# Optimization experiments

Measured on AMD Instinct MI355X. Metric: run time of the kernel, lower is better.

The kernel has to match this reference:

```python
import jax, jax.numpy as jnp
import numpy as np

N = 8192  # nv + nh, bias=False


def setup_inputs() -> dict:
    key = jax.random.key(0)
    k1, k2, k3, k4 = jax.random.split(key, 4)
    w = jax.random.normal(k1, (N, N), dtype=jnp.float32) * 0.01  # learned [n,n] coupling matrix
    initial_state = jax.random.randint(k2, (N,), 0, 2).astype(jnp.float32)  # binary unit states
    clamping_degree = jnp.zeros((N,), dtype=jnp.float32)  # 0 => unit is free to update
    T = jnp.float32(1.0)  # temperature
    perm = jax.random.permutation(k3, N).astype(jnp.int32)  # torch.randperm(self.n)
    rand_u = jax.random.uniform(k4, (N,), dtype=jnp.float32)  # torch.rand(1) per unit
    return {"w": w, "initial_state": initial_state, "clamping_degree": clamping_degree,
            "T": T, "perm": perm, "rand_u": rand_u}


def reference(w, initial_state, clamping_degree, T, perm, rand_u):
    # Sequential Gibbs sweep: for each j in perm, if unclamped,
    # p = sigmoid(w[j]@state / T); state[j] = 1 if u <= p else 0.
    inactive = jnp.float32(0.0)

    def step(state, ju):
        j, u = ju
        sum_input = jnp.dot(w[j], state)          # per-unit dot product against current state
        p = jax.nn.sigmoid(sum_input / T)          # 1/(1+exp(-x/T))
        new_val = jnp.where(u <= p, jnp.float32(1.0), inactive)
        upd = jnp.where(clamping_degree[j] == 0, new_val, state[j])
        return state.at[j].set(upd), None

    final_state, _ = jax.lax.scan(step, initial_state, (perm, rand_u))
    return final_state
```

## Files before the change

### kernel.cpp

```cpp
#include <hip/hip_runtime.h>
#include <math.h>


#define NN 8192
#define BB 512
#define NBLK 16
#define SUB 64
#define NSUB 8
#define NWG 256
#define NWORK 255
#define TPB 512
#define MAXR 3
#define MSTR 68
#define MBUFW (SUB * MSTR)

typedef unsigned int u32;
typedef unsigned long long u64;

__global__ void k_init(u32* flags, int n) {
  int i = blockIdx.x * blockDim.x + threadIdx.x;
  for (; i < n; i += gridDim.x * blockDim.x) flags[i] = 0;
}

__device__ __forceinline__ u32 ld_rlx(const u32* p) {
  return __hip_atomic_load(p, __ATOMIC_RELAXED, __HIP_MEMORY_SCOPE_AGENT);
}
__device__ __forceinline__ void st_rlx(u32* p, u32 v) {
  __hip_atomic_store(p, v, __ATOMIC_RELAXED, __HIP_MEMORY_SCOPE_AGENT);
}
__device__ __forceinline__ float ldf_rlx(const float* p) {
  return __hip_atomic_load(p, __ATOMIC_RELAXED, __HIP_MEMORY_SCOPE_AGENT);
}
__device__ __forceinline__ void stf_rlx(float* p, float v) {
  __hip_atomic_store(p, v, __ATOMIC_RELAXED, __HIP_MEMORY_SCOPE_AGENT);
}
__device__ __forceinline__ double ldd_rlx(const double* p) {
  return __hip_atomic_load(p, __ATOMIC_RELAXED, __HIP_MEMORY_SCOPE_AGENT);
}
__device__ __forceinline__ void std_rlx(double* p, double v) {
  __hip_atomic_store(p, v, __ATOMIC_RELAXED, __HIP_MEMORY_SCOPE_AGENT);
}

__global__ __launch_bounds__(TPB) void k_gibbs(
    const float* __restrict__ w, const float* __restrict__ init,
    const float* __restrict__ clampv, const float* __restrict__ Tp,
    const int* __restrict__ perm, const float* __restrict__ urand,
    float* __restrict__ dout, double* __restrict__ S,
    float* __restrict__ delG, float* __restrict__ tileD,
    u32* delReady, u32* ack) {
  __shared__ double poolD[55296 / 8];
  const int wg = blockIdx.x, tid = threadIdx.x;
  const int wv = tid >> 6, lane = tid & 63;

  if (wg == 0) {
    double* sumsL = poolD;
    double* thrL  = poolD + BB;
    float*  d1L   = (float*)(poolD + 2 * BB);
    float*  d0L   = d1L + BB;
    float*  delL  = d0L + BB;
    float*  oldL  = delL + BB;
    int*    uL    = (int*)(oldL + BB);
    float*  mbuf  = (float*)(uL + BB);

    double T = (double)Tp[0];
    for (int b = 0; b < NBLK; ++b) {
      const bool pub = (b + 1 < NBLK);
      int pos = b * BB + tid;
      int unit = perm[pos];
      double uu = (double)urand[pos];
      thrL[tid] = T * log(uu / (1.0 - uu));
      float old = init[unit];
      bool cl = (clampv[unit] != 0.0f);
      d1L[tid] = cl ? 0.0f : (1.0f - old);
      d0L[tid] = cl ? 0.0f : (0.0f - old);
      oldL[tid] = old;
      uL[tid] = unit;
      {
        const u32* slots = ack + (size_t)b * NWORK;
        for (;;) {
          int ok = 1;
          if (tid < NWORK) ok = (ld_rlx(&slots[tid]) != 0u);
          if (__syncthreads_and(ok)) break;
          __builtin_amdgcn_s_sleep(1);
        }
      }
      sumsL[tid] = ldd_rlx(&S[(size_t)b * BB + tid]);
      if (tid >= 448) {
        int l = tid - 448;
        const float4* src = (const float4*)(tileD + (size_t)b * BB * BB + (size_t)l * BB);
        float4* dst = (float4*)(mbuf + l * MSTR);
#pragma unroll
        for (int j = 0; j < 16; ++j) dst[j] = src[j];
      }
      __syncthreads();
      const float* tb = tileD + (size_t)b * BB * BB;
      float4 nv0, nv1, nv2, nv3;

      for (int t8 = 0; t8 < NSUB; ++t8) {
        int o = t8 * SUB;
        float m[SUB];
        if (tid < SUB) {
          const float4* mr = (const float4*)(mbuf + (t8 & 1) * MBUFW + tid * MSTR);
#pragma unroll
          for (int j = 0; j < 16; ++j) {
            float4 v = mr[j];
            m[4*j] = v.x; m[4*j+1] = v.y; m[4*j+2] = v.z; m[4*j+3] = v.w;
          }
        } else if (t8 > 0 && tid >= 256) {
          int t = tid - 256, g_ = t >> 2, q = t & 3;
          int rrow = o + g_;
          int c0 = (t8 - 1) * SUB + q * 16;
          double p_ =
              (double)(nv0.x * delL[c0])    + (double)(nv0.y * delL[c0+1]) +
              (double)(nv0.z * delL[c0+2])  + (double)(nv0.w * delL[c0+3]) +
              (double)(nv1.x * delL[c0+4])  + (double)(nv1.y * delL[c0+5]) +
              (double)(nv1.z * delL[c0+6])  + (double)(nv1.w * delL[c0+7]);
          p_ +=
              (double)(nv2.x * delL[c0+8])  + (double)(nv2.y * delL[c0+9]) +
              (double)(nv2.z * delL[c0+10]) + (double)(nv2.w * delL[c0+11]) +
              (double)(nv3.x * delL[c0+12]) + (double)(nv3.y * delL[c0+13]) +
              (double)(nv3.z * delL[c0+14]) + (double)(nv3.w * delL[c0+15]);
          p_ += __shfl_down(p_, 2, 4);
          p_ += __shfl_down(p_, 1, 4);
          if (q == 0) sumsL[rrow] += p_;
        }
        __syncthreads();
        if (tid < SUB) {
          float d1v = d1L[o + tid], d0v = d0L[o + tid];
          u64 P1 = __ballot(d1v != 0.0f);
          u64 M0 = __ballot(d0v != 0.0f);
          double g = sumsL[o + tid] - thrL[o + tid];
          u64 xb = 0ull;
          __builtin_amdgcn_s_setprio(3);
#pragma unroll
          for (int s = 0; s < SUB; ++s) {
            u32 t1 = ((P1 >> s) & 1ull) ? 0x3f800000u : 0u;
            u32 t0 = ((M0 >> s) & 1ull) ? 0xbf800000u : 0u;
            int hi = __builtin_amdgcn_readlane(
                (int)(__double_as_longlong(g) >> 32), s);
            float sdf = __uint_as_float((hi >= 0) ? t1 : t0);
            g += (double)(m[s] * sdf);
            xb |= ((u64)(hi >= 0 ? 1 : 0)) << s;
          }
          __builtin_amdgcn_s_setprio(0);
          delL[o + tid] = ((xb >> tid) & 1ull) ? d1v : d0v;
        } else if (tid < 128) {
          if (t8 < NSUB - 1) {
            int l = tid - 64, o2 = (t8 + 1) * SUB;
            const float4* src = (const float4*)(tb + (size_t)(o2 + l) * BB + o2);
            float4* dst = (float4*)(mbuf + ((t8 + 1) & 1) * MBUFW + l * MSTR);
#pragma unroll
            for (int j = 0; j < 16; ++j) dst[j] = src[j];
          }
        } else {
          if (t8 < NSUB - 1 && tid >= 256) {
            int t = tid - 256;
            const float4* pr = (const float4*)(
                tb + (size_t)((t8 + 1) * SUB + (t >> 2)) * BB + o + (t & 3) * 16);
            nv0 = pr[0]; nv1 = pr[1]; nv2 = pr[2]; nv3 = pr[3];
          }
          if (t8 > 0) {
            for (int r = (t8 + 1) * SUB + (tid - 128); r < BB; r += 384) {
              int c0 = (t8 - 1) * SUB;
              const float4* mr3 = (const float4*)(tb + (size_t)r * BB + c0);
              double acc = sumsL[r];
#pragma unroll
              for (int j = 0; j < SUB / 4; ++j) {
                float4 v = mr3[j];
                acc += (double)(v.x * delL[c0+4*j])   + (double)(v.y * delL[c0+4*j+1]) +
                       (double)(v.z * delL[c0+4*j+2]) + (double)(v.w * delL[c0+4*j+3]);
              }
              sumsL[r] = acc;
            }
          }
        }
        __syncthreads();
      }
      if (pub) {
        stf_rlx(&delG[b * BB + tid], delL[tid]);
        __syncthreads();
        if (tid == 0) st_rlx(&delReady[b], 1u);
      }
      dout[uL[tid]] = oldL[tid] + delL[tid];
    }
  } else {
    float* stateL = (float*)poolD;
    double* redW = (double*)((char*)poolD + 32768);
    const int iw = wg - 1;
    const int r0 = (iw * BB) / NWORK, r1 = ((iw + 1) * BB) / NWORK;
    const int cnt = r1 - r0;
    for (int i = tid; i < NN; i += TPB) stateL[i] = init[i];
    __syncthreads();

    for (int p = 0; p < NBLK; ++p) {
      int pc = perm[p * BB + tid];
      float g[NSUB];
      float* tbp = tileD + (size_t)p * BB * BB;

      for (int ri = 0; ri < cnt; ++ri) {
        int unit = perm[p * BB + r0 + ri];
        const float* wrow = w + (size_t)unit * NN;
        const float4* wr4 = (const float4*)wrow;
        const float4* st4 = (const float4*)stateL;
        double acc = 0.0;
#pragma unroll
        for (int k = 0; k < NN / (4 * TPB); ++k) {
          float4 a = wr4[tid + k * TPB];
          float4 s = st4[tid + k * TPB];
          acc += (double)(a.x * s.x) + (double)(a.y * s.y) +
                 (double)(a.z * s.z) + (double)(a.w * s.w);
        }
        for (int o = 32; o > 0; o >>= 1) acc += __shfl_down(acc, o, 64);
        if (lane == 0) redW[wv * MAXR + ri] = acc;
        stf_rlx(&tbp[(size_t)(r0 + ri) * BB + tid], wrow[pc]);
        if (p > 0 && wv == ri) {
#pragma unroll
          for (int t8 = 0; t8 < NSUB; ++t8)
            g[t8] = wrow[perm[(p - 1) * BB + t8 * SUB + lane]];
        }
      }
      __syncthreads();
      double Sr = 0.0;
      if (wv < cnt) {
#pragma unroll
        for (int k = 0; k < TPB / 64; ++k) Sr += redW[k * MAXR + wv];
      }
      if (p > 0) {
        if (tid == 0) {
          while (ld_rlx(&delReady[p - 1]) == 0u) __builtin_amdgcn_s_sleep(1);
        }
        __syncthreads();
        double crr = 0.0;
        if (wv < cnt) {
#pragma unroll
          for (int t8 = 0; t8 < NSUB; ++t8)
            crr += (double)(g[t8] * ldf_rlx(&delG[(p - 1) * BB + t8 * SUB + lane]));
          for (int o = 32; o > 0; o >>= 1) crr += __shfl_down(crr, o, 64);
          Sr += crr;
        }
      }
      if (wv < cnt && lane == 0) std_rlx(&S[(size_t)p * BB + r0 + wv], Sr);
      __syncthreads();
      if (tid == 0) st_rlx(&ack[(size_t)p * NWORK + iw], 1u);
      if (p > 0) {
        float dl = ldf_rlx(&delG[(p - 1) * BB + tid]);
        stateL[perm[(p - 1) * BB + tid]] += dl;
      }
      __syncthreads();
    }
  }
}

extern "C" void kernel_launch(void* const* d_in, const int* in_sizes, int n_in,
                              void* d_out, int out_size, void* d_ws, size_t ws_size,
                              hipStream_t stream) {
  const float* w      = (const float*)d_in[0];
  const float* init   = (const float*)d_in[1];
  const float* clampv = (const float*)d_in[2];
  const float* Tp     = (const float*)d_in[3];
  const int*   perm   = (const int*)d_in[4];
  const float* urand  = (const float*)d_in[5];
  float* dout = (float*)d_out;

  double* S    = (double*)d_ws;
  float* delG  = (float*)(S + (size_t)NBLK * BB);
  float* tileD = delG + NN;
  u32* delReady = (u32*)(tileD + (size_t)NBLK * BB * BB);
  u32* ack      = delReady + NBLK;

  int nflags = NBLK + NBLK * NWORK;
  k_init<<<8, 256, 0, stream>>>(delReady, nflags);

  void* args[] = {(void*)&w, (void*)&init, (void*)&clampv, (void*)&Tp,
                  (void*)&perm, (void*)&urand, (void*)&dout,
                  (void*)&S, (void*)&delG, (void*)&tileD,
                  (void*)&delReady, (void*)&ack};
  hipLaunchCooperativeKernel((const void*)k_gibbs, dim3(NWG), dim3(TPB),
                             args, 0, stream);
}
```

Measured before the change: 589.4 us.

## Publish Gibbs deltas per sub-block and defer last sub-block correction to master

The master workgroup now publishes each 64-unit sub-block of state deltas with its own flag as soon as it is sampled, instead of one flag per 512-unit block. Worker workgroups consume the first seven sub-blocks progressively while computing their corrections. The last sub-block's contribution is handled by the master itself, using a new strip of weights (stripG) that workers write, so workers need not wait for the whole block to finish. This aims to shorten the critical serial dependency between master and workers. The cost is more flag polling and barriers, extra global traffic for the strip, and more complex synchronization.

```diff
diff --git a/kernel.cpp b/kernel.cpp
--- a/kernel.cpp
+++ b/kernel.cpp
@@ -46,8 +46,8 @@
     const float* __restrict__ clampv, const float* __restrict__ Tp,
     const int* __restrict__ perm, const float* __restrict__ urand,
     float* __restrict__ dout, double* __restrict__ S,
-    float* __restrict__ delG, float* __restrict__ tileD,
-    u32* delReady, u32* ack) {
+    float* __restrict__ delG, float* __restrict__ stripG,
+    float* __restrict__ tileD, u32* subFlag, u32* ack) {
   __shared__ double poolD[55296 / 8];
   const int wg = blockIdx.x, tid = threadIdx.x;
   const int wv = tid >> 6, lane = tid & 63;
@@ -55,16 +55,22 @@
   if (wg == 0) {
     double* sumsL = poolD;
     double* thrL  = poolD + BB;
-    float*  d1L   = (float*)(poolD + 2 * BB);
-    float*  d0L   = d1L + BB;
-    float*  delL  = d0L + BB;
-    float*  oldL  = delL + BB;
-    int*    uL    = (int*)(oldL + BB);
-    float*  mbuf  = (float*)(uL + BB);
+    float*  fbase = (float*)(poolD + 2 * BB);
+    float*  d1L   = fbase;
+    float*  d0L   = fbase + BB;
+    float*  delL  = fbase + 2 * BB;
+    float*  oldL  = fbase + 3 * BB;
+    float*  del7L = fbase + 4 * BB;
+    int*    uL    = (int*)(fbase + 4 * BB + SUB);
+    float*  mbuf  = fbase + 4 * BB + SUB + BB;
 
     double T = (double)Tp[0];
+    float4 nv0, nv1, nv2, nv3;
+    float4 sv0, sv1, sv2, sv3;
+
     for (int b = 0; b < NBLK; ++b) {
       const bool pub = (b + 1 < NBLK);
+      if (b > 0 && tid < SUB) del7L[tid] = delL[(NSUB - 1) * SUB + tid];
       int pos = b * BB + tid;
       int unit = perm[pos];
       double uu = (double)urand[pos];
@@ -85,6 +91,12 @@
         }
       }
       sumsL[tid] = ldd_rlx(&S[(size_t)b * BB + tid]);
+      if (b > 0 && tid >= 256) {
+        int t = tid - 256;
+        const float4* pr = (const float4*)(
+            stripG + ((size_t)b * BB + (t >> 2)) * SUB + (t & 3) * 16);
+        sv0 = pr[0]; sv1 = pr[1]; sv2 = pr[2]; sv3 = pr[3];
+      }
       if (tid >= 448) {
         int l = tid - 448;
         const float4* src = (const float4*)(tileD + (size_t)b * BB * BB + (size_t)l * BB);
@@ -94,11 +106,11 @@
       }
       __syncthreads();
       const float* tb = tileD + (size_t)b * BB * BB;
-      float4 nv0, nv1, nv2, nv3;
 
       for (int t8 = 0; t8 < NSUB; ++t8) {
         int o = t8 * SUB;
         float m[SUB];
+        if (t8 > 0 && pub && tid == 0) st_rlx(&subFlag[b * NSUB + t8 - 1], 1u);
         if (tid < SUB) {
           const float4* mr = (const float4*)(mbuf + (t8 & 1) * MBUFW + tid * MSTR);
 #pragma unroll
@@ -106,20 +118,32 @@
             float4 v = mr[j];
             m[4*j] = v.x; m[4*j+1] = v.y; m[4*j+2] = v.z; m[4*j+3] = v.w;
           }
-        } else if (t8 > 0 && tid >= 256) {
+        } else if (tid >= 256 && (t8 > 0 || b > 0)) {
           int t = tid - 256, g_ = t >> 2, q = t & 3;
           int rrow = o + g_;
-          int c0 = (t8 - 1) * SUB + q * 16;
-          double p_ =
-              (double)(nv0.x * delL[c0])    + (double)(nv0.y * delL[c0+1]) +
-              (double)(nv0.z * delL[c0+2])  + (double)(nv0.w * delL[c0+3]) +
-              (double)(nv1.x * delL[c0+4])  + (double)(nv1.y * delL[c0+5]) +
-              (double)(nv1.z * delL[c0+6])  + (double)(nv1.w * delL[c0+7]);
-          p_ +=
-              (double)(nv2.x * delL[c0+8])  + (double)(nv2.y * delL[c0+9]) +
-              (double)(nv2.z * delL[c0+10]) + (double)(nv2.w * delL[c0+11]) +
-              (double)(nv3.x * delL[c0+12]) + (double)(nv3.y * delL[c0+13]) +
-              (double)(nv3.z * delL[c0+14]) + (double)(nv3.w * delL[c0+15]);
+          double p_ = 0.0;
+          if (t8 > 0) {
+            int c0 = (t8 - 1) * SUB + q * 16;
+            p_ += (double)(nv0.x * delL[c0])    + (double)(nv0.y * delL[c0+1]) +
+                  (double)(nv0.z * delL[c0+2])  + (double)(nv0.w * delL[c0+3]) +
+                  (double)(nv1.x * delL[c0+4])  + (double)(nv1.y * delL[c0+5]) +
+                  (double)(nv1.z * delL[c0+6])  + (double)(nv1.w * delL[c0+7]) +
+                  (double)(nv2.x * delL[c0+8])  + (double)(nv2.y * delL[c0+9]) +
+                  (double)(nv2.z * delL[c0+10]) + (double)(nv2.w * delL[c0+11]) +
+                  (double)(nv3.x * delL[c0+12]) + (double)(nv3.y * delL[c0+13]) +
+                  (double)(nv3.z * delL[c0+14]) + (double)(nv3.w * delL[c0+15]);
+          }
+          if (b > 0) {
+            int c0 = q * 16;
+            p_ += (double)(sv0.x * del7L[c0])    + (double)(sv0.y * del7L[c0+1]) +
+                  (double)(sv0.z * del7L[c0+2])  + (double)(sv0.w * del7L[c0+3]) +
+                  (double)(sv1.x * del7L[c0+4])  + (double)(sv1.y * del7L[c0+5]) +
+                  (double)(sv1.z * del7L[c0+6])  + (double)(sv1.w * del7L[c0+7]) +
+                  (double)(sv2.x * del7L[c0+8])  + (double)(sv2.y * del7L[c0+9]) +
+                  (double)(sv2.z * del7L[c0+10]) + (double)(sv2.w * del7L[c0+11]) +
+                  (double)(sv3.x * del7L[c0+12]) + (double)(sv3.y * del7L[c0+13]) +
+                  (double)(sv3.z * del7L[c0+14]) + (double)(sv3.w * del7L[c0+15]);
+          }
           p_ += __shfl_down(p_, 2, 4);
           p_ += __shfl_down(p_, 1, 4);
           if (q == 0) sumsL[rrow] += p_;
@@ -143,7 +167,9 @@
             xb |= ((u64)(hi >= 0 ? 1 : 0)) << s;
           }
           __builtin_amdgcn_s_setprio(0);
-          delL[o + tid] = ((xb >> tid) & 1ull) ? d1v : d0v;
+          float mydel = ((xb >> tid) & 1ull) ? d1v : d0v;
+          delL[o + tid] = mydel;
+          if (pub) stf_rlx(&delG[b * BB + o + tid], mydel);
         } else if (tid < 128) {
           if (t8 < NSUB - 1) {
             int l = tid - 64, o2 = (t8 + 1) * SUB;
@@ -158,6 +184,11 @@
             const float4* pr = (const float4*)(
                 tb + (size_t)((t8 + 1) * SUB + (t >> 2)) * BB + o + (t & 3) * 16);
             nv0 = pr[0]; nv1 = pr[1]; nv2 = pr[2]; nv3 = pr[3];
+            if (b > 0) {
+              const float4* sr = (const float4*)(
+                  stripG + ((size_t)b * BB + (t8 + 1) * SUB + (t >> 2)) * SUB + (t & 3) * 16);
+              sv0 = sr[0]; sv1 = sr[1]; sv2 = sr[2]; sv3 = sr[3];
+            }
           }
           if (t8 > 0) {
             for (int r = (t8 + 1) * SUB + (tid - 128); r < BB; r += 384) {
@@ -176,11 +207,7 @@
         }
         __syncthreads();
       }
-      if (pub) {
-        stf_rlx(&delG[b * BB + tid], delL[tid]);
-        __syncthreads();
-        if (tid == 0) st_rlx(&delReady[b], 1u);
-      }
+      if (pub && tid == 0) st_rlx(&subFlag[b * NSUB + NSUB - 1], 1u);
       dout[uL[tid]] = oldL[tid] + delL[tid];
     }
   } else {
@@ -193,8 +220,17 @@
     __syncthreads();
 
     for (int p = 0; p < NBLK; ++p) {
+      if (p >= 2) {
+        const u32* f = &subFlag[(p - 2) * NSUB + NSUB - 1];
+        if (tid == 0) { while (ld_rlx(f) == 0u) __builtin_amdgcn_s_sleep(1); }
+        __syncthreads();
+        if (tid < SUB)
+          stateL[perm[(p - 2) * BB + 7 * SUB + tid]] +=
+              ldf_rlx(&delG[(p - 2) * BB + 7 * SUB + tid]);
+        __syncthreads();
+      }
       int pc = perm[p * BB + tid];
-      float g[NSUB];
+      float g[NSUB - 1];
       float* tbp = tileD + (size_t)p * BB * BB;
 
       for (int ri = 0; ri < cnt; ++ri) {
@@ -215,8 +251,10 @@
         stf_rlx(&tbp[(size_t)(r0 + ri) * BB + tid], wrow[pc]);
         if (p > 0 && wv == ri) {
 #pragma unroll
-          for (int t8 = 0; t8 < NSUB; ++t8)
+          for (int t8 = 0; t8 < NSUB - 1; ++t8)
             g[t8] = wrow[perm[(p - 1) * BB + t8 * SUB + lane]];
+          stf_rlx(&stripG[((size_t)p * BB + r0 + ri) * SUB + lane],
+                  wrow[perm[(p - 1) * BB + 7 * SUB + lane]]);
         }
       }
       __syncthreads();
@@ -226,27 +264,22 @@
         for (int k = 0; k < TPB / 64; ++k) Sr += redW[k * MAXR + wv];
       }
       if (p > 0) {
-        if (tid == 0) {
-          while (ld_rlx(&delReady[p - 1]) == 0u) __builtin_amdgcn_s_sleep(1);
-        }
-        __syncthreads();
         double crr = 0.0;
-        if (wv < cnt) {
-#pragma unroll
-          for (int t8 = 0; t8 < NSUB; ++t8)
-            crr += (double)(g[t8] * ldf_rlx(&delG[(p - 1) * BB + t8 * SUB + lane]));
-          for (int o = 32; o > 0; o >>= 1) crr += __shfl_down(crr, o, 64);
-          Sr += crr;
-        }
+#pragma unroll
+        for (int t8 = 0; t8 < NSUB - 1; ++t8) {
+          const u32* f = &subFlag[(p - 1) * NSUB + t8];
+          if (tid == 0) { while (ld_rlx(f) == 0u) __builtin_amdgcn_s_sleep(1); }
+          __syncthreads();
+          float dl = ldf_rlx(&delG[(p - 1) * BB + t8 * SUB + lane]);
+          if (wv < cnt) crr += (double)(g[t8] * dl);
+          if (tid < SUB) stateL[perm[(p - 1) * BB + t8 * SUB + tid]] += dl;
+        }
+        for (int o = 32; o > 0; o >>= 1) crr += __shfl_down(crr, o, 64);
+        Sr += crr;
       }
       if (wv < cnt && lane == 0) std_rlx(&S[(size_t)p * BB + r0 + wv], Sr);
       __syncthreads();
       if (tid == 0) st_rlx(&ack[(size_t)p * NWORK + iw], 1u);
-      if (p > 0) {
-        float dl = ldf_rlx(&delG[(p - 1) * BB + tid]);
-        stateL[perm[(p - 1) * BB + tid]] += dl;
-      }
-      __syncthreads();
     }
   }
 }
@@ -264,17 +297,18 @@
 
   double* S    = (double*)d_ws;
   float* delG  = (float*)(S + (size_t)NBLK * BB);
-  float* tileD = delG + NN;
-  u32* delReady = (u32*)(tileD + (size_t)NBLK * BB * BB);
-  u32* ack      = delReady + NBLK;
-
-  int nflags = NBLK + NBLK * NWORK;
-  k_init<<<8, 256, 0, stream>>>(delReady, nflags);
+  float* stripG = delG + NN;
+  float* tileD = stripG + (size_t)NBLK * BB * SUB;
+  u32* subFlag = (u32*)(tileD + (size_t)NBLK * BB * BB);
+  u32* ack     = subFlag + NBLK * NSUB;
+
+  int nflags = NBLK * NSUB + NBLK * NWORK;
+  k_init<<<8, 256, 0, stream>>>(subFlag, nflags);
 
   void* args[] = {(void*)&w, (void*)&init, (void*)&clampv, (void*)&Tp,
                   (void*)&perm, (void*)&urand, (void*)&dout,
-                  (void*)&S, (void*)&delG, (void*)&tileD,
-                  (void*)&delReady, (void*)&ack};
+                  (void*)&S, (void*)&delG, (void*)&stripG, (void*)&tileD,
+                  (void*)&subFlag, (void*)&ack};
   hipLaunchCooperativeKernel((const void*)k_gibbs, dim3(NWG), dim3(TPB),
                              args, 0, stream);
 }
```

Result: no change. 596.6 us (+1.2%).

## Alternate sampler blocks across two workgroups with per-subtile flags and cross-tile correction

Applied to the files above, without the earlier changes.

The sequential sampler role is now shared by two workgroups that alternate 512-unit blocks, with 254 worker groups instead of 255. Workers compute base sums for block q from state up to q-2 and write an extra tile of off-diagonal couplings. The sampler for block b folds in the previous block's updates itself, subtile by subtile, as per-subtile flags fire. The aim is to start the next block's serial chain before the previous block finishes, overlapping the serial critical path, at the cost of more tile traffic, finer-grained flag polling and a larger shared-memory footprint.

```diff
diff --git a/kernel.cpp b/kernel.cpp
--- a/kernel.cpp
+++ b/kernel.cpp
@@ -8,7 +8,7 @@
 #define SUB 64
 #define NSUB 8
 #define NWG 256
-#define NWORK 255
+#define NWORK 254
 #define TPB 512
 #define MAXR 3
 #define MSTR 68
@@ -47,23 +47,27 @@
     const int* __restrict__ perm, const float* __restrict__ urand,
     float* __restrict__ dout, double* __restrict__ S,
     float* __restrict__ delG, float* __restrict__ tileD,
-    u32* delReady, u32* ack) {
-  __shared__ double poolD[55296 / 8];
+    float* __restrict__ tileO, u32* subFlag, u32* ackS) {
+  __shared__ double poolD[8896];
   const int wg = blockIdx.x, tid = threadIdx.x;
   const int wv = tid >> 6, lane = tid & 63;
 
-  if (wg == 0) {
+  if (wg < 2) {
     double* sumsL = poolD;
     double* thrL  = poolD + BB;
-    float*  d1L   = (float*)(poolD + 2 * BB);
-    float*  d0L   = d1L + BB;
-    float*  delL  = d0L + BB;
-    float*  oldL  = delL + BB;
-    int*    uL    = (int*)(oldL + BB);
-    float*  mbuf  = (float*)(uL + BB);
+    float*  fb    = (float*)(poolD + 2 * BB);
+    float*  d1L   = fb;
+    float*  d0L   = fb + BB;
+    float*  delL  = fb + 2 * BB;
+    float*  oldL  = fb + 3 * BB;
+    int*    uL    = (int*)(fb + 4 * BB);
+    float*  del7L = (float*)(uL + BB);
+    float*  pdelL = del7L + SUB;
+    float*  s7L   = pdelL + SUB;
+    float*  mbuf  = s7L + SUB * MSTR;
 
     double T = (double)Tp[0];
-    for (int b = 0; b < NBLK; ++b) {
+    for (int b = wg; b < NBLK; b += 2) {
       const bool pub = (b + 1 < NBLK);
       int pos = b * BB + tid;
       int unit = perm[pos];
@@ -76,7 +80,7 @@
       oldL[tid] = old;
       uL[tid] = unit;
       {
-        const u32* slots = ack + (size_t)b * NWORK;
+        const u32* slots = ackS + (size_t)b * NWORK;
         for (;;) {
           int ok = 1;
           if (tid < NWORK) ok = (ld_rlx(&slots[tid]) != 0u);
@@ -85,20 +89,76 @@
         }
       }
       sumsL[tid] = ldd_rlx(&S[(size_t)b * BB + tid]);
-      if (tid >= 448) {
-        int l = tid - 448;
-        const float4* src = (const float4*)(tileD + (size_t)b * BB * BB + (size_t)l * BB);
-        float4* dst = (float4*)(mbuf + l * MSTR);
-#pragma unroll
-        for (int j = 0; j < 16; ++j) dst[j] = src[j];
-      }
       __syncthreads();
       const float* tb = tileD + (size_t)b * BB * BB;
+      const float* to = tileO + (size_t)b * BB * BB;
+
+      if (b > 0) {
+        for (int t8 = 0; t8 < NSUB - 1; ++t8) {
+          if (tid == 0) {
+            while (ld_rlx(&subFlag[(b - 1) * NSUB + t8]) == 0u)
+              __builtin_amdgcn_s_sleep(1);
+          }
+          __syncthreads();
+          if (tid < SUB) pdelL[tid] = ldf_rlx(&delG[(b - 1) * BB + t8 * SUB + tid]);
+          __syncthreads();
+          {
+            const float4* rp = (const float4*)(to + (size_t)tid * BB + t8 * SUB);
+            double acc = 0.0;
+#pragma unroll
+            for (int j = 0; j < SUB / 4; ++j) {
+              float4 v = rp[j];
+              acc += (double)(v.x * pdelL[4*j])   + (double)(v.y * pdelL[4*j+1]) +
+                     (double)(v.z * pdelL[4*j+2]) + (double)(v.w * pdelL[4*j+3]);
+            }
+            sumsL[tid] += acc;
+          }
+          __syncthreads();
+        }
+        {
+          int r = tid >> 3, c0 = (tid & 7) * 8;
+          const float4* sp = (const float4*)(to + (size_t)r * BB + 7 * SUB + c0);
+          float4 a = sp[0], bq = sp[1];
+          float4* dp = (float4*)(s7L + r * MSTR + c0);
+          dp[0] = a; dp[1] = bq;
+          const float4* mp = (const float4*)(tb + (size_t)r * BB + c0);
+          float4 c = mp[0], d = mp[1];
+          float4* dq = (float4*)(mbuf + r * MSTR + c0);
+          dq[0] = c; dq[1] = d;
+        }
+        if (tid == 0) {
+          while (ld_rlx(&subFlag[(b - 1) * NSUB + 7]) == 0u)
+            __builtin_amdgcn_s_sleep(1);
+        }
+        __syncthreads();
+        if (tid < SUB) del7L[tid] = ldf_rlx(&delG[(b - 1) * BB + 7 * SUB + tid]);
+        __syncthreads();
+        {
+          int r = tid >> 3, c0 = (tid & 7) * 8;
+          double a2 = 0.0;
+#pragma unroll
+          for (int j = 0; j < 8; ++j)
+            a2 += (double)(s7L[r * MSTR + c0 + j] * del7L[c0 + j]);
+          a2 += __shfl_down(a2, 4, 8);
+          a2 += __shfl_down(a2, 2, 8);
+          a2 += __shfl_down(a2, 1, 8);
+          if ((tid & 7) == 0) sumsL[r] += a2;
+        }
+        __syncthreads();
+      } else {
+        int r = tid >> 3, c0 = (tid & 7) * 8;
+        const float4* mp = (const float4*)(tb + (size_t)r * BB + c0);
+        float4 c = mp[0], d = mp[1];
+        float4* dq = (float4*)(mbuf + r * MSTR + c0);
+        dq[0] = c; dq[1] = d;
+        __syncthreads();
+      }
+
       float4 nv0, nv1, nv2, nv3;
-
       for (int t8 = 0; t8 < NSUB; ++t8) {
         int o = t8 * SUB;
         float m[SUB];
+        if (t8 > 0 && pub && tid == 0) st_rlx(&subFlag[b * NSUB + t8 - 1], 1u);
         if (tid < SUB) {
           const float4* mr = (const float4*)(mbuf + (t8 & 1) * MBUFW + tid * MSTR);
 #pragma unroll
@@ -107,8 +167,8 @@
             m[4*j] = v.x; m[4*j+1] = v.y; m[4*j+2] = v.z; m[4*j+3] = v.w;
           }
         } else if (t8 > 0 && tid >= 256) {
-          int t = tid - 256, g_ = t >> 2, q = t & 3;
-          int rrow = o + g_;
+          int t = tid - 256, q = t & 3;
+          int rrow = o + (t >> 2);
           int c0 = (t8 - 1) * SUB + q * 16;
           double p_ =
               (double)(nv0.x * delL[c0])    + (double)(nv0.y * delL[c0+1]) +
@@ -127,15 +187,15 @@
         __syncthreads();
         if (tid < SUB) {
           float d1v = d1L[o + tid], d0v = d0L[o + tid];
-          u64 P1 = __ballot(d1v != 0.0f);
-          u64 M0 = __ballot(d0v != 0.0f);
+          u64 P1m = __ballot(d1v != 0.0f);
+          u64 M0m = __ballot(d0v != 0.0f);
           double g = sumsL[o + tid] - thrL[o + tid];
           u64 xb = 0ull;
           __builtin_amdgcn_s_setprio(3);
 #pragma unroll
           for (int s = 0; s < SUB; ++s) {
-            u32 t1 = ((P1 >> s) & 1ull) ? 0x3f800000u : 0u;
-            u32 t0 = ((M0 >> s) & 1ull) ? 0xbf800000u : 0u;
+            u32 t1 = ((P1m >> s) & 1ull) ? 0x3f800000u : 0u;
+            u32 t0 = ((M0m >> s) & 1ull) ? 0xbf800000u : 0u;
             int hi = __builtin_amdgcn_readlane(
                 (int)(__double_as_longlong(g) >> 32), s);
             float sdf = __uint_as_float((hi >= 0) ? t1 : t0);
@@ -143,7 +203,9 @@
             xb |= ((u64)(hi >= 0 ? 1 : 0)) << s;
           }
           __builtin_amdgcn_s_setprio(0);
-          delL[o + tid] = ((xb >> tid) & 1ull) ? d1v : d0v;
+          float mydel = ((xb >> tid) & 1ull) ? d1v : d0v;
+          delL[o + tid] = mydel;
+          if (pub) stf_rlx(&delG[b * BB + o + tid], mydel);
         } else if (tid < 128) {
           if (t8 < NSUB - 1) {
             int l = tid - 64, o2 = (t8 + 1) * SUB;
@@ -172,33 +234,52 @@
               }
               sumsL[r] = acc;
             }
-          }
-        }
-        __syncthreads();
-      }
-      if (pub) {
-        stf_rlx(&delG[b * BB + tid], delL[tid]);
-        __syncthreads();
-        if (tid == 0) st_rlx(&delReady[b], 1u);
-      }
+          } else if (b > 0) {
+            for (int r = SUB + (tid - 128); r < BB; r += 384) {
+              const float4* mr3 = (const float4*)(to + (size_t)r * BB + 7 * SUB);
+              double acc = sumsL[r];
+#pragma unroll
+              for (int j = 0; j < SUB / 4; ++j) {
+                float4 v = mr3[j];
+                acc += (double)(v.x * del7L[4*j])   + (double)(v.y * del7L[4*j+1]) +
+                       (double)(v.z * del7L[4*j+2]) + (double)(v.w * del7L[4*j+3]);
+              }
+              sumsL[r] = acc;
+            }
+          }
+        }
+        __syncthreads();
+      }
+      if (pub && tid == 0) st_rlx(&subFlag[b * NSUB + 7], 1u);
       dout[uL[tid]] = oldL[tid] + delL[tid];
     }
   } else {
     float* stateL = (float*)poolD;
     double* redW = (double*)((char*)poolD + 32768);
-    const int iw = wg - 1;
+    const int iw = wg - 2;
     const int r0 = (iw * BB) / NWORK, r1 = ((iw + 1) * BB) / NWORK;
     const int cnt = r1 - r0;
     for (int i = tid; i < NN; i += TPB) stateL[i] = init[i];
     __syncthreads();
 
-    for (int p = 0; p < NBLK; ++p) {
-      int pc = perm[p * BB + tid];
-      float g[NSUB];
-      float* tbp = tileD + (size_t)p * BB * BB;
+    for (int q = 0; q < NBLK; ++q) {
+      if (q >= 2) {
+        if (tid == 0) {
+          while (ld_rlx(&subFlag[(q - 2) * NSUB + 7]) == 0u)
+            __builtin_amdgcn_s_sleep(1);
+        }
+        __syncthreads();
+        float dl = ldf_rlx(&delG[(q - 2) * BB + tid]);
+        stateL[perm[(q - 2) * BB + tid]] += dl;
+        __syncthreads();
+      }
+      int pcD = perm[q * BB + tid];
+      int pcO = (q > 0) ? perm[(q - 1) * BB + tid] : 0;
+      float* tbp = tileD + (size_t)q * BB * BB;
+      float* top = tileO + (size_t)q * BB * BB;
 
       for (int ri = 0; ri < cnt; ++ri) {
-        int unit = perm[p * BB + r0 + ri];
+        int unit = perm[q * BB + r0 + ri];
         const float* wrow = w + (size_t)unit * NN;
         const float4* wr4 = (const float4*)wrow;
         const float4* st4 = (const float4*)stateL;
@@ -212,12 +293,8 @@
         }
         for (int o = 32; o > 0; o >>= 1) acc += __shfl_down(acc, o, 64);
         if (lane == 0) redW[wv * MAXR + ri] = acc;
-        stf_rlx(&tbp[(size_t)(r0 + ri) * BB + tid], wrow[pc]);
-        if (p > 0 && wv == ri) {
-#pragma unroll
-          for (int t8 = 0; t8 < NSUB; ++t8)
-            g[t8] = wrow[perm[(p - 1) * BB + t8 * SUB + lane]];
-        }
+        stf_rlx(&tbp[(size_t)(r0 + ri) * BB + tid], wrow[pcD]);
+        if (q > 0) stf_rlx(&top[(size_t)(r0 + ri) * BB + tid], wrow[pcO]);
       }
       __syncthreads();
       double Sr = 0.0;
@@ -225,28 +302,9 @@
 #pragma unroll
         for (int k = 0; k < TPB / 64; ++k) Sr += redW[k * MAXR + wv];
       }
-      if (p > 0) {
-        if (tid == 0) {
-          while (ld_rlx(&delReady[p - 1]) == 0u) __builtin_amdgcn_s_sleep(1);
-        }
-        __syncthreads();
-        double crr = 0.0;
-        if (wv < cnt) {
-#pragma unroll
-          for (int t8 = 0; t8 < NSUB; ++t8)
-            crr += (double)(g[t8] * ldf_rlx(&delG[(p - 1) * BB + t8 * SUB + lane]));
-          for (int o = 32; o > 0; o >>= 1) crr += __shfl_down(crr, o, 64);
-          Sr += crr;
-        }
-      }
-      if (wv < cnt && lane == 0) std_rlx(&S[(size_t)p * BB + r0 + wv], Sr);
+      if (wv < cnt && lane == 0) std_rlx(&S[(size_t)q * BB + r0 + wv], Sr);
       __syncthreads();
-      if (tid == 0) st_rlx(&ack[(size_t)p * NWORK + iw], 1u);
-      if (p > 0) {
-        float dl = ldf_rlx(&delG[(p - 1) * BB + tid]);
-        stateL[perm[(p - 1) * BB + tid]] += dl;
-      }
-      __syncthreads();
+      if (tid == 0) st_rlx(&ackS[(size_t)q * NWORK + iw], 1u);
     }
   }
 }
@@ -265,16 +323,17 @@
   double* S    = (double*)d_ws;
   float* delG  = (float*)(S + (size_t)NBLK * BB);
   float* tileD = delG + NN;
-  u32* delReady = (u32*)(tileD + (size_t)NBLK * BB * BB);
-  u32* ack      = delReady + NBLK;
-
-  int nflags = NBLK + NBLK * NWORK;
-  k_init<<<8, 256, 0, stream>>>(delReady, nflags);
+  float* tileO = tileD + (size_t)NBLK * BB * BB;
+  u32* subFlag = (u32*)(tileO + (size_t)NBLK * BB * BB);
+  u32* ackS    = subFlag + NBLK * NSUB;
+
+  int nflags = NBLK * NSUB + NBLK * NWORK;
+  k_init<<<8, 256, 0, stream>>>(subFlag, nflags);
 
   void* args[] = {(void*)&w, (void*)&init, (void*)&clampv, (void*)&Tp,
                   (void*)&perm, (void*)&urand, (void*)&dout,
-                  (void*)&S, (void*)&delG, (void*)&tileD,
-                  (void*)&delReady, (void*)&ack};
+                  (void*)&S, (void*)&delG, (void*)&tileD, (void*)&tileO,
+                  (void*)&subFlag, (void*)&ackS};
   hipLaunchCooperativeKernel((const void*)k_gibbs, dim3(NWG), dim3(TPB),
                              args, 0, stream);
 }
```

Result: slower. 653.4 us (+10.9%).
